# Performance work log

Measured on AMD Instinct MI355X. Metric: run time of the kernel, lower is better.

The kernel has to match this reference:

```python
import jax, jax.numpy as jnp
import numpy as np

N, NNODES, CIN, COUT = 64, 512, 32, 64


def setup_inputs() -> dict:
    key = jax.random.key(0)
    k1, k2, k3, k4, k5 = jax.random.split(key, 5)
    A = jax.random.normal(k1, (N, NNODES, NNODES), dtype=jnp.float32)
    X = jax.random.normal(k2, (N, NNODES, CIN), dtype=jnp.float32)
    A_coeffs = jax.random.normal(k3, (5 + 2 * CIN,), dtype=jnp.float32)
    x_num = 4 + 2 * CIN
    scale = np.sqrt(2.0) / (COUT + x_num)
    X_coeffs_1 = jax.random.normal(k4, (COUT, x_num), dtype=jnp.float32) * scale
    X_coeffs_2 = jax.random.normal(k5, (COUT, x_num), dtype=jnp.float32) * scale
    return {"A": A, "X": X, "A_coeffs": A_coeffs,
            "X_coeffs_1": X_coeffs_1, "X_coeffs_2": X_coeffs_2}


def _forward(A, X, A_coeffs, W1, W2):
    n = A.shape[-1]
    C = X.shape[-1]
    Xt = jnp.swapaxes(X, -1, -2)                      # N,C,n
    diag = jnp.diagonal(A, axis1=-2, axis2=-1)        # N,n
    mean_diag = diag.mean(-1)                         # N
    mean_cols = A.mean(-1)                            # N,n
    mean_all = mean_cols.mean(-1)                     # N
    mean_X = Xt.mean(-1)                              # N,C

    c = A_coeffs
    w6 = c[5:5 + C]                                   # coeffs for a6 (X_i + X_j)
    w7 = c[5 + C:5 + 2 * C]                           # coeffs for a7 (mean_X)
    # Fold the 'd,ndij->nij' contraction over the 7 basis tensors into
    # scalar/row/col broadcast terms (identical math, no N x (5+2C) x n x n tensor).
    s = jnp.einsum('c,nci->ni', w6, Xt)               # N,n
    const = c[1] * mean_all + c[2] * mean_diag + jnp.einsum('c,nc->n', w7, mean_X)
    vec = c[3] * mean_cols + c[4] * diag + s          # N,n
    A_t = c[0] * A + const[:, None, None] + vec[:, :, None] + vec[:, None, :]

    # X basis out_x: N x (4+2C) x n, order [x1, x2, x3, x4, x5, x6]
    ones_n = jnp.ones((1, 1, n), A.dtype)
    out_x = jnp.concatenate([
        Xt,                                           # x1: N,C,n
        mean_X[:, :, None] * ones_n,                  # x2: N,C,n
        mean_cols[:, None, :],                        # x3: N,1,n
        diag[:, None, :],                             # x4: N,1,n
        mean_diag[:, None, None] * ones_n,            # x5: N,1,n
        mean_all[:, None, None] * ones_n,             # x6: N,1,n
    ], axis=1)
    X1 = jnp.einsum('bd,ndi->nbi', W1, out_x)         # N,B,n
    X2 = jnp.einsum('bd,ndi->nbi', W2, out_x)         # N,B,n
    out = jnp.einsum('nij,nbj->nbi', A_t, X1) / n + X2  # N,B,n
    return jnp.swapaxes(out, -1, -2)                  # N,n,B


def reference(A, X, A_coeffs, X_coeffs_1, X_coeffs_2):
    return _forward(A, X, A_coeffs, X_coeffs_1, X_coeffs_2)
```

## Files before the change

kernel.cpp:

```cpp
#include <hip/hip_runtime.h>
#include <hip/hip_bf16.h>

#define NB 64
#define NN 512
#define CI 32
#define CO 64
#define XN 68

typedef __attribute__((ext_vector_type(8))) short bf16x8;
typedef __attribute__((ext_vector_type(4))) float f32x4;

__device__ inline short f2bf(float f) {
  union { __hip_bfloat16 h; unsigned short u; } cv;
  cv.h = __float2bfloat16(f);
  return (short)cv.u;
}

__device__ inline bf16x8 cvt8(float4 a, float4 b) {
  bf16x8 r;
  r[0] = f2bf(a.x); r[1] = f2bf(a.y); r[2] = f2bf(a.z); r[3] = f2bf(a.w);
  r[4] = f2bf(b.x); r[5] = f2bf(b.y); r[6] = f2bf(b.z); r[7] = f2bf(b.w);
  return r;
}

__device__ inline bf16x8 cvt8s(float4 a, float4 b, float s) {
  bf16x8 r;
  r[0] = f2bf(a.x * s); r[1] = f2bf(a.y * s); r[2] = f2bf(a.z * s); r[3] = f2bf(a.w * s);
  r[4] = f2bf(b.x * s); r[5] = f2bf(b.y * s); r[6] = f2bf(b.z * s); r[7] = f2bf(b.w * s);
  return r;
}

__global__ __launch_bounds__(256) void k1_rowstats(
    const float* __restrict__ A, float* __restrict__ mc, float* __restrict__ dg,
    float* __restrict__ pA, float* __restrict__ pD) {
  int b = blockIdx.x, ch = blockIdx.y;
  int t = threadIdx.x, w = t >> 6, lane = t & 63;
  int r0 = ch * 16;
  const float* Ab = A + (size_t)b * NN * NN;
  __shared__ float wsum[4];
  __shared__ float sD[16];
  float4 v0[4], v1[4];
#pragma unroll
  for (int m = 0; m < 4; ++m) {
    const float* rp = Ab + (size_t)(r0 + w * 4 + m) * NN;
    v0[m] = *(const float4*)(rp + lane * 4);
    v1[m] = *(const float4*)(rp + 256 + lane * 4);
  }
  float accR = 0.f;
#pragma unroll
  for (int m = 0; m < 4; ++m) {
    float s = (v0[m].x + v0[m].y) + (v0[m].z + v0[m].w) +
              (v1[m].x + v1[m].y) + (v1[m].z + v1[m].w);
#pragma unroll
    for (int off = 1; off < 64; off <<= 1) s += __shfl_xor(s, off, 64);
    if (lane == 0) mc[b * NN + r0 + w * 4 + m] = s * (1.0f / NN);
    accR += s;
  }
  if (lane == 0) wsum[w] = accR;
  if (t < 16) {
    float d = Ab[(size_t)(r0 + t) * NN + r0 + t];
    dg[b * NN + r0 + t] = d;
    sD[t] = d;
  }
  __syncthreads();
  if (t == 0) {
    pA[b * 32 + ch] = wsum[0] + wsum[1] + wsum[2] + wsum[3];
    float sd = 0.f;
#pragma unroll
    for (int k = 0; k < 16; ++k) sd += sD[k];
    pD[b * 32 + ch] = sd;
  }
}

__global__ __launch_bounds__(512) void k2_merged(
    const float* __restrict__ X, const float* __restrict__ cf,
    const float* __restrict__ W1, const float* __restrict__ W2,
    const float* __restrict__ mc, const float* __restrict__ dg,
    const float* __restrict__ pA, const float* __restrict__ pD,
    float* __restrict__ vplus, float* __restrict__ colv,
    unsigned short* __restrict__ X1) {
  int b = blockIdx.x, t = threadIdx.x;
  int w = t >> 6, lane = t & 63;
  __shared__ float sX[NN][36];
  __shared__ float sSv[NN];
  __shared__ float sMXp[16][32], sTCp[16][32];
  __shared__ float sWr[8][3];
  __shared__ float sc[69], mX[CI], tC[CI], sA1[CO];
  __shared__ float sS[6];

  if (t < 69) sc[t] = cf[t];
  const float* Xb = X + (size_t)b * NN * CI;
  float4 x4[8];
#pragma unroll
  for (int k = 0; k < 8; ++k) {
    x4[k] = *(const float4*)(Xb + (size_t)t * CI + k * 4);
    *(float4*)&sX[t][k * 4] = x4[k];
  }
  float mcj = mc[b * NN + t], dgj = dg[b * NN + t];
  __syncthreads();
  float sv = 0.f;
#pragma unroll
  for (int k = 0; k < 8; ++k) {
    sv += sc[5 + k * 4] * x4[k].x + sc[6 + k * 4] * x4[k].y +
          sc[7 + k * 4] * x4[k].z + sc[8 + k * 4] * x4[k].w;
  }
  float svec = fmaf(sc[3], mcj, fmaf(sc[4], dgj, sv));
  sSv[t] = svec;
  float p1 = svec, p2 = svec * mcj, p3 = svec * dgj;
#pragma unroll
  for (int off = 1; off < 64; off <<= 1) {
    p1 += __shfl_xor(p1, off, 64);
    p2 += __shfl_xor(p2, off, 64);
    p3 += __shfl_xor(p3, off, 64);
  }
  if (lane == 0) { sWr[w][0] = p1; sWr[w][1] = p2; sWr[w][2] = p3; }
  __syncthreads();
  {
    int c = lane & 31, rg = w * 2 + (lane >> 5);
    float s1 = 0.f, s2 = 0.f;
#pragma unroll
    for (int r = 0; r < 32; ++r) {
      int j = rg * 32 + r;
      float v = sX[j][c];
      s1 += v;
      s2 += sSv[j] * v;
    }
    sMXp[rg][c] = s1;
    sTCp[rg][c] = s2;
  }
  __syncthreads();
  if (t < 32) {
    float s1 = 0.f, s2 = 0.f;
#pragma unroll
    for (int g = 0; g < 16; ++g) { s1 += sMXp[g][t]; s2 += sTCp[g][t]; }
    mX[t] = s1 * (1.0f / NN);
    tC[t] = s2;
  } else if (t == 32) {
    float sA = 0.f, sD = 0.f;
#pragma unroll
    for (int k = 0; k < 32; ++k) { sA += pA[b * 32 + k]; sD += pD[b * 32 + k]; }
    sS[0] = sD * (1.0f / NN);
    sS[1] = sA * (1.0f / ((float)NN * (float)NN));
  } else if (t == 33) {
    float s1 = 0.f, s2 = 0.f, s3 = 0.f;
#pragma unroll
    for (int k = 0; k < 8; ++k) { s1 += sWr[k][0]; s2 += sWr[k][1]; s3 += sWr[k][2]; }
    sS[3] = s1; sS[4] = s2; sS[5] = s3;
  }
  __syncthreads();
  if (t == 0) {
    float s7 = 0.f;
#pragma unroll
    for (int c = 0; c < CI; ++c) s7 += sc[5 + CI + c] * mX[c];
    sS[2] = sc[1] * sS[1] + sc[2] * sS[0] + s7;
  }
  __syncthreads();
  vplus[b * NN + t] = sSv[t] + sS[2];
  if (t < CO) {
    int o = t;
    const float* w1 = W1 + o * XN;
    const float* w2 = W2 + o * XN;
    float w1mX = 0.f, a1 = 0.f, a2 = 0.f, wt = 0.f;
#pragma unroll
    for (int c = 0; c < CI; ++c) {
      w1mX += w1[c] * mX[c];
      a1 += w1[CI + c] * mX[c];
      a2 += w2[CI + c] * mX[c];
      wt += w1[c] * tC[c];
    }
    float smd = sS[0], sma = sS[1];
    a1 += w1[66] * smd + w1[67] * sma;
    a2 += w2[66] * smd + w2[67] * sma;
    float we0 = w1[64], we1 = w1[65];
    float S1n = w1mX + a1 + we0 * sma + we1 * smd;
    float SVn = (wt + a1 * sS[3] + we0 * sS[4] + we1 * sS[5]) * (1.0f / NN);
    sA1[o] = a1;
    float4 cvv = make_float4(S1n, a2 + SVn, w2[64], w2[65]);
    *(float4*)&colv[(b * CO + o) * 4] = cvv;
  }
  __syncthreads();
  {
    int ra = lane & 15, kg = lane >> 4, g = lane >> 4;
    bf16x8 wfrag[4];
    float ao[4], e0[4], e1[4];
#pragma unroll
    for (int to = 0; to < 4; ++to) {
      int o = to * 16 + ra;
      const float* wp = W1 + o * XN + kg * 8;
      wfrag[to] = cvt8(*(const float4*)wp, *(const float4*)(wp + 4));
      ao[to] = sA1[o];
      e0[to] = W1[o * XN + 64];
      e1[to] = W1[o * XN + 65];
    }
#pragma unroll
    for (int jj = 0; jj < 4; ++jj) {
      int j0 = w * 64 + jj * 16;
      const float* xp = &sX[j0 + ra][kg * 8];
      bf16x8 xf = cvt8(*(const float4*)xp, *(const float4*)(xp + 4));
      float4 mcv = *(const float4*)&mc[b * NN + j0 + g * 4];
      float4 dgv = *(const float4*)&dg[b * NN + j0 + g * 4];
      float mcr[4] = {mcv.x, mcv.y, mcv.z, mcv.w};
      float dgr[4] = {dgv.x, dgv.y, dgv.z, dgv.w};
#pragma unroll
      for (int to = 0; to < 4; ++to) {
        f32x4 zero = {0.f, 0.f, 0.f, 0.f};
        f32x4 d = __builtin_amdgcn_mfma_f32_16x16x32_bf16(xf, wfrag[to], zero, 0, 0, 0);
        union { unsigned short u[4]; uint2 v; } pk;
#pragma unroll
        for (int r = 0; r < 4; ++r) {
          float val = d[r] + ao[to] + e0[to] * mcr[r] + e1[to] * dgr[r];
          pk.u[r] = (unsigned short)f2bf(val);
        }
        *(uint2*)(X1 + ((size_t)b * CO + to * 16 + ra) * NN + j0 + g * 4) = pk.v;
      }
    }
  }
}

__global__ __launch_bounds__(512) void k5_mfma(
    const float* __restrict__ A, const unsigned short* __restrict__ X1,
    const float* __restrict__ X, const float* __restrict__ W2,
    const float* __restrict__ vplus, const float* __restrict__ mc,
    const float* __restrict__ dg, const float* __restrict__ colv,
    const float* __restrict__ cf, float* __restrict__ out) {
  int b = blockIdx.x, ic = blockIdx.y;
  int t = threadIdx.x, w = t >> 6, lane = t & 63;
  int ia = w & 1, q = w >> 1;
  int ra = lane & 15, kg = lane >> 4, g = lane >> 4;
  int i0 = ic * 32;
  __shared__ float sAcc[4 * 32 * 68];

  float c0n = cf[0] * (1.0f / NN);
  const float* Arow = A + ((size_t)(b * NN + i0 + ia * 16 + ra)) * NN;
  const unsigned short* X1b = X1 + (size_t)b * CO * NN;

  f32x4 acc[4] = {{0.f, 0.f, 0.f, 0.f}, {0.f, 0.f, 0.f, 0.f},
                  {0.f, 0.f, 0.f, 0.f}, {0.f, 0.f, 0.f, 0.f}};

#pragma unroll
  for (int jt = 0; jt < 4; ++jt) {
    int kb = q * 128 + jt * 32 + kg * 8;
    float4 a0 = *(const float4*)(Arow + kb);
    float4 a1 = *(const float4*)(Arow + kb + 4);
    bf16x8 af = cvt8s(a0, a1, c0n);
#pragma unroll
    for (int to = 0; to < 4; ++to) {
      bf16x8 bf = *(const bf16x8*)(X1b + (size_t)(to * 16 + ra) * NN + kb);
      acc[to] = __builtin_amdgcn_mfma_f32_16x16x32_bf16(af, bf, acc[to], 0, 0, 0);
    }
  }

  if (q == 0) {
    const float* xp = X + (size_t)(b * NN + i0 + ia * 16 + ra) * CI + kg * 8;
    bf16x8 xf = cvt8(*(const float4*)xp, *(const float4*)(xp + 4));
#pragma unroll
    for (int to = 0; to < 4; ++to) {
      const float* wp = W2 + (size_t)(to * 16 + ra) * XN + kg * 8;
      bf16x8 wf = cvt8(*(const float4*)wp, *(const float4*)(wp + 4));
      acc[to] = __builtin_amdgcn_mfma_f32_16x16x32_bf16(xf, wf, acc[to], 0, 0, 0);
    }
  }

  int ei = t >> 4, eo4 = (t & 15) * 4;
  float e_vp = vplus[b * NN + i0 + ei];
  float e_mc = mc[b * NN + i0 + ei];
  float e_dg = dg[b * NN + i0 + ei];
  float4 cv0 = *(const float4*)&colv[(b * CO + eo4 + 0) * 4];
  float4 cv1 = *(const float4*)&colv[(b * CO + eo4 + 1) * 4];
  float4 cv2 = *(const float4*)&colv[(b * CO + eo4 + 2) * 4];
  float4 cv3 = *(const float4*)&colv[(b * CO + eo4 + 3) * 4];

#pragma unroll
  for (int to = 0; to < 4; ++to)
#pragma unroll
    for (int r = 0; r < 4; ++r)
      sAcc[(q * 32 + ia * 16 + g * 4 + r) * 68 + to * 16 + ra] = acc[to][r];
  __syncthreads();

  {
    f32x4 s = {0.f, 0.f, 0.f, 0.f};
#pragma unroll
    for (int qq = 0; qq < 4; ++qq) s += *(const f32x4*)&sAcc[(qq * 32 + ei) * 68 + eo4];
    float4 res;
    res.x = s[0] + e_vp * cv0.x + cv0.y + e_mc * cv0.z + e_dg * cv0.w;
    res.y = s[1] + e_vp * cv1.x + cv1.y + e_mc * cv1.z + e_dg * cv1.w;
    res.z = s[2] + e_vp * cv2.x + cv2.y + e_mc * cv2.z + e_dg * cv2.w;
    res.w = s[3] + e_vp * cv3.x + cv3.y + e_mc * cv3.z + e_dg * cv3.w;
    *(float4*)&out[((size_t)(b * NN + i0 + ei)) * CO + eo4] = res;
  }
}

extern "C" void kernel_launch(void* const* d_in, const int* in_sizes, int n_in,
                              void* d_out, int out_size, void* d_ws, size_t ws_size,
                              hipStream_t stream) {
  const float* A = (const float*)d_in[0];
  const float* X = (const float*)d_in[1];
  const float* cf = (const float*)d_in[2];
  const float* W1 = (const float*)d_in[3];
  const float* W2 = (const float*)d_in[4];
  float* out = (float*)d_out;

  float* p = (float*)d_ws;
  float* mc = p;      p += NB * NN;
  float* dg = p;      p += NB * NN;
  float* vplus = p;   p += NB * NN;
  float* pA = p;      p += NB * 32;
  float* pD = p;      p += NB * 32;
  float* colv = p;    p += NB * CO * 4;
  unsigned short* X1 = (unsigned short*)p;

  k1_rowstats<<<dim3(NB, 32), 256, 0, stream>>>(A, mc, dg, pA, pD);
  k2_merged<<<NB, 512, 0, stream>>>(X, cf, W1, W2, mc, dg, pA, pD,
                                    vplus, colv, X1);
  k5_mfma<<<dim3(NB, 16), 512, 0, stream>>>(A, X1, X, W2, vplus, mc, dg,
                                            colv, cf, out);
}
```

Before: 55.71 us.

## Split X1 projection into separate kernel and fold mean/diag terms into extra MFMA rows

Moves the X·W1 MFMA projection out of the single-block-per-batch stats kernel into a new kernel with a 64x4 grid, so the projection no longer depends on the A row statistics. The mean_cols and diag contributions are no longer baked into X1. Instead they are stored as two extra bf16 rows of an extended Y buffer and contracted against A with one more MFMA per tile in the main kernel, then combined in the epilogue using per-output coefficients. The stats kernel now uses 1024 threads with shuffle reductions instead of LDS staging. This adds a fourth kernel launch and extra MFMA and global traffic for the padded rows.

New measurement: 68.89 us. 1.24x slower.

```diff
diff --git a/kernel.cpp b/kernel.cpp
--- a/kernel.cpp
+++ b/kernel.cpp
@@ -6,6 +6,7 @@
 #define CI 32
 #define CO 64
 #define XN 68
+#define YR 80
 
 typedef __attribute__((ext_vector_type(8))) short bf16x8;
 typedef __attribute__((ext_vector_type(4))) float f32x4;
@@ -72,61 +73,110 @@
   }
 }
 
-__global__ __launch_bounds__(512) void k2_merged(
+__global__ __launch_bounds__(256) void kY(
+    const float* __restrict__ X, const float* __restrict__ W1,
+    unsigned short* __restrict__ Yext) {
+  int b = blockIdx.x, yc = blockIdx.y;
+  int t = threadIdx.x, w = t >> 6, lane = t & 63;
+  int ra = lane & 15, kg = lane >> 4, g = lane >> 4;
+  const float* Xb = X + (size_t)b * NN * CI;
+
+  bf16x8 wfrag[4];
+#pragma unroll
+  for (int to = 0; to < 4; ++to) {
+    const float* wp = W1 + (to * 16 + ra) * XN + kg * 8;
+    wfrag[to] = cvt8(*(const float4*)wp, *(const float4*)(wp + 4));
+  }
+#pragma unroll
+  for (int jj = 0; jj < 2; ++jj) {
+    int j0 = yc * 128 + w * 32 + jj * 16;
+    const float* xp = Xb + (size_t)(j0 + ra) * CI + kg * 8;
+    bf16x8 xf = cvt8(*(const float4*)xp, *(const float4*)(xp + 4));
+#pragma unroll
+    for (int to = 0; to < 4; ++to) {
+      f32x4 zero = {0.f, 0.f, 0.f, 0.f};
+      f32x4 d = __builtin_amdgcn_mfma_f32_16x16x32_bf16(xf, wfrag[to], zero, 0, 0, 0);
+      union { unsigned short u[4]; uint2 v; } pk;
+#pragma unroll
+      for (int r = 0; r < 4; ++r) pk.u[r] = (unsigned short)f2bf(d[r]);
+      *(uint2*)(Yext + ((size_t)b * YR + to * 16 + ra) * NN + j0 + g * 4) = pk.v;
+    }
+  }
+  for (int idx = t; idx < 14 * 32; idx += 256) {
+    int row = 66 + (idx >> 5);
+    int c4 = (idx & 31) * 4;
+    *(uint2*)(Yext + ((size_t)b * YR + row) * NN + yc * 128 + c4) = make_uint2(0u, 0u);
+  }
+}
+
+__global__ __launch_bounds__(1024) void k2_stats(
     const float* __restrict__ X, const float* __restrict__ cf,
     const float* __restrict__ W1, const float* __restrict__ W2,
     const float* __restrict__ mc, const float* __restrict__ dg,
     const float* __restrict__ pA, const float* __restrict__ pD,
     float* __restrict__ vplus, float* __restrict__ colv,
-    unsigned short* __restrict__ X1) {
+    unsigned short* __restrict__ Yext) {
   int b = blockIdx.x, t = threadIdx.x;
   int w = t >> 6, lane = t & 63;
-  __shared__ float sX[NN][36];
-  __shared__ float sSv[NN];
-  __shared__ float sMXp[16][32], sTCp[16][32];
-  __shared__ float sWr[8][3];
-  __shared__ float sc[69], mX[CI], tC[CI], sA1[CO];
+  int h = t & 1, j = t >> 1;
+  __shared__ float sMXp[16][32], sTCp[16][32], sP[16][3];
+  __shared__ float sc[69], mX[CI], tC[CI];
   __shared__ float sS[6];
 
   if (t < 69) sc[t] = cf[t];
-  const float* Xb = X + (size_t)b * NN * CI;
-  float4 x4[8];
-#pragma unroll
-  for (int k = 0; k < 8; ++k) {
-    x4[k] = *(const float4*)(Xb + (size_t)t * CI + k * 4);
-    *(float4*)&sX[t][k * 4] = x4[k];
-  }
-  float mcj = mc[b * NN + t], dgj = dg[b * NN + t];
-  __syncthreads();
-  float sv = 0.f;
-#pragma unroll
-  for (int k = 0; k < 8; ++k) {
-    sv += sc[5 + k * 4] * x4[k].x + sc[6 + k * 4] * x4[k].y +
-          sc[7 + k * 4] * x4[k].z + sc[8 + k * 4] * x4[k].w;
-  }
-  float svec = fmaf(sc[3], mcj, fmaf(sc[4], dgj, sv));
-  sSv[t] = svec;
-  float p1 = svec, p2 = svec * mcj, p3 = svec * dgj;
+  const float* xp = X + ((size_t)b * NN + j) * CI + h * 16;
+  float4 x4[4];
+#pragma unroll
+  for (int k = 0; k < 4; ++k) x4[k] = *(const float4*)(xp + k * 4);
+  float mcj = mc[b * NN + j], dgj = dg[b * NN + j];
+  __syncthreads();
+
+  float up = 0.f;
+#pragma unroll
+  for (int k = 0; k < 4; ++k) {
+    int c0 = 5 + h * 16 + k * 4;
+    up += sc[c0] * x4[k].x + sc[c0 + 1] * x4[k].y +
+          sc[c0 + 2] * x4[k].z + sc[c0 + 3] * x4[k].w;
+  }
+  float u = up + __shfl_xor(up, 1, 64);
+  float vec = fmaf(sc[3], mcj, fmaf(sc[4], dgj, u));
+
+  float p1 = h ? 0.f : vec;
+  float p2 = h ? 0.f : vec * mcj;
+  float p3 = h ? 0.f : vec * dgj;
+  float4 t4[4];
+#pragma unroll
+  for (int k = 0; k < 4; ++k) {
+    t4[k].x = vec * x4[k].x; t4[k].y = vec * x4[k].y;
+    t4[k].z = vec * x4[k].z; t4[k].w = vec * x4[k].w;
+  }
 #pragma unroll
   for (int off = 1; off < 64; off <<= 1) {
     p1 += __shfl_xor(p1, off, 64);
     p2 += __shfl_xor(p2, off, 64);
     p3 += __shfl_xor(p3, off, 64);
   }
-  if (lane == 0) { sWr[w][0] = p1; sWr[w][1] = p2; sWr[w][2] = p3; }
-  __syncthreads();
-  {
-    int c = lane & 31, rg = w * 2 + (lane >> 5);
-    float s1 = 0.f, s2 = 0.f;
-#pragma unroll
-    for (int r = 0; r < 32; ++r) {
-      int j = rg * 32 + r;
-      float v = sX[j][c];
-      s1 += v;
-      s2 += sSv[j] * v;
-    }
-    sMXp[rg][c] = s1;
-    sTCp[rg][c] = s2;
+#pragma unroll
+  for (int off = 2; off < 64; off <<= 1) {
+#pragma unroll
+    for (int k = 0; k < 4; ++k) {
+      x4[k].x += __shfl_xor(x4[k].x, off, 64);
+      x4[k].y += __shfl_xor(x4[k].y, off, 64);
+      x4[k].z += __shfl_xor(x4[k].z, off, 64);
+      x4[k].w += __shfl_xor(x4[k].w, off, 64);
+      t4[k].x += __shfl_xor(t4[k].x, off, 64);
+      t4[k].y += __shfl_xor(t4[k].y, off, 64);
+      t4[k].z += __shfl_xor(t4[k].z, off, 64);
+      t4[k].w += __shfl_xor(t4[k].w, off, 64);
+    }
+  }
+  if (lane < 2) {
+#pragma unroll
+    for (int k = 0; k < 4; ++k) {
+      *(float4*)&sMXp[w][lane * 16 + k * 4] = x4[k];
+      *(float4*)&sTCp[w][lane * 16 + k * 4] = t4[k];
+    }
+    if (lane == 0) { sP[w][0] = p1; sP[w][1] = p2; sP[w][2] = p3; }
   }
   __syncthreads();
   if (t < 32) {
@@ -144,7 +194,7 @@
   } else if (t == 33) {
     float s1 = 0.f, s2 = 0.f, s3 = 0.f;
 #pragma unroll
-    for (int k = 0; k < 8; ++k) { s1 += sWr[k][0]; s2 += sWr[k][1]; s3 += sWr[k][2]; }
+    for (int k = 0; k < 16; ++k) { s1 += sP[k][0]; s2 += sP[k][1]; s3 += sP[k][2]; }
     sS[3] = s1; sS[4] = s2; sS[5] = s3;
   }
   __syncthreads();
@@ -155,7 +205,13 @@
     sS[2] = sc[1] * sS[1] + sc[2] * sS[0] + s7;
   }
   __syncthreads();
-  vplus[b * NN + t] = sSv[t] + sS[2];
+  if (h == 0) vplus[b * NN + j] = vec + sS[2];
+  if (t < NN) {
+    Yext[((size_t)b * YR + 64) * NN + t] = (unsigned short)f2bf(mc[b * NN + t]);
+  } else {
+    int t2 = t - NN;
+    Yext[((size_t)b * YR + 65) * NN + t2] = (unsigned short)f2bf(dg[b * NN + t2]);
+  }
   if (t < CO) {
     int o = t;
     const float* w1 = W1 + o * XN;
@@ -174,51 +230,15 @@
     float we0 = w1[64], we1 = w1[65];
     float S1n = w1mX + a1 + we0 * sma + we1 * smd;
     float SVn = (wt + a1 * sS[3] + we0 * sS[4] + we1 * sS[5]) * (1.0f / NN);
-    sA1[o] = a1;
-    float4 cvv = make_float4(S1n, a2 + SVn, w2[64], w2[65]);
-    *(float4*)&colv[(b * CO + o) * 4] = cvv;
-  }
-  __syncthreads();
-  {
-    int ra = lane & 15, kg = lane >> 4, g = lane >> 4;
-    bf16x8 wfrag[4];
-    float ao[4], e0[4], e1[4];
-#pragma unroll
-    for (int to = 0; to < 4; ++to) {
-      int o = to * 16 + ra;
-      const float* wp = W1 + o * XN + kg * 8;
-      wfrag[to] = cvt8(*(const float4*)wp, *(const float4*)(wp + 4));
-      ao[to] = sA1[o];
-      e0[to] = W1[o * XN + 64];
-      e1[to] = W1[o * XN + 65];
-    }
-#pragma unroll
-    for (int jj = 0; jj < 4; ++jj) {
-      int j0 = w * 64 + jj * 16;
-      const float* xp = &sX[j0 + ra][kg * 8];
-      bf16x8 xf = cvt8(*(const float4*)xp, *(const float4*)(xp + 4));
-      float4 mcv = *(const float4*)&mc[b * NN + j0 + g * 4];
-      float4 dgv = *(const float4*)&dg[b * NN + j0 + g * 4];
-      float mcr[4] = {mcv.x, mcv.y, mcv.z, mcv.w};
-      float dgr[4] = {dgv.x, dgv.y, dgv.z, dgv.w};
-#pragma unroll
-      for (int to = 0; to < 4; ++to) {
-        f32x4 zero = {0.f, 0.f, 0.f, 0.f};
-        f32x4 d = __builtin_amdgcn_mfma_f32_16x16x32_bf16(xf, wfrag[to], zero, 0, 0, 0);
-        union { unsigned short u[4]; uint2 v; } pk;
-#pragma unroll
-        for (int r = 0; r < 4; ++r) {
-          float val = d[r] + ao[to] + e0[to] * mcr[r] + e1[to] * dgr[r];
-          pk.u[r] = (unsigned short)f2bf(val);
-        }
-        *(uint2*)(X1 + ((size_t)b * CO + to * 16 + ra) * NN + j0 + g * 4) = pk.v;
-      }
-    }
+    float4 cva = make_float4(S1n, a2 + SVn, w2[64] + sc[0] * a1, w2[65]);
+    float4 cvb = make_float4(we0, we1, 0.f, 0.f);
+    *(float4*)&colv[(b * CO + o) * 8] = cva;
+    *(float4*)&colv[(b * CO + o) * 8 + 4] = cvb;
   }
 }
 
 __global__ __launch_bounds__(512) void k5_mfma(
-    const float* __restrict__ A, const unsigned short* __restrict__ X1,
+    const float* __restrict__ A, const unsigned short* __restrict__ Yext,
     const float* __restrict__ X, const float* __restrict__ W2,
     const float* __restrict__ vplus, const float* __restrict__ mc,
     const float* __restrict__ dg, const float* __restrict__ colv,
@@ -229,13 +249,15 @@
   int ra = lane & 15, kg = lane >> 4, g = lane >> 4;
   int i0 = ic * 32;
   __shared__ float sAcc[4 * 32 * 68];
+  __shared__ float sG[4 * 32 * 2];
 
   float c0n = cf[0] * (1.0f / NN);
   const float* Arow = A + ((size_t)(b * NN + i0 + ia * 16 + ra)) * NN;
-  const unsigned short* X1b = X1 + (size_t)b * CO * NN;
+  const unsigned short* Yb = Yext + (size_t)b * YR * NN;
 
   f32x4 acc[4] = {{0.f, 0.f, 0.f, 0.f}, {0.f, 0.f, 0.f, 0.f},
                   {0.f, 0.f, 0.f, 0.f}, {0.f, 0.f, 0.f, 0.f}};
+  f32x4 acc4 = {0.f, 0.f, 0.f, 0.f};
 
 #pragma unroll
   for (int jt = 0; jt < 4; ++jt) {
@@ -245,9 +267,11 @@
     bf16x8 af = cvt8s(a0, a1, c0n);
 #pragma unroll
     for (int to = 0; to < 4; ++to) {
-      bf16x8 bf = *(const bf16x8*)(X1b + (size_t)(to * 16 + ra) * NN + kb);
+      bf16x8 bf = *(const bf16x8*)(Yb + (size_t)(to * 16 + ra) * NN + kb);
       acc[to] = __builtin_amdgcn_mfma_f32_16x16x32_bf16(af, bf, acc[to], 0, 0, 0);
     }
+    bf16x8 bf4 = *(const bf16x8*)(Yb + (size_t)(64 + ra) * NN + kb);
+    acc4 = __builtin_amdgcn_mfma_f32_16x16x32_bf16(af, bf4, acc4, 0, 0, 0);
   }
 
   if (q == 0) {
@@ -265,27 +289,41 @@
   float e_vp = vplus[b * NN + i0 + ei];
   float e_mc = mc[b * NN + i0 + ei];
   float e_dg = dg[b * NN + i0 + ei];
-  float4 cv0 = *(const float4*)&colv[(b * CO + eo4 + 0) * 4];
-  float4 cv1 = *(const float4*)&colv[(b * CO + eo4 + 1) * 4];
-  float4 cv2 = *(const float4*)&colv[(b * CO + eo4 + 2) * 4];
-  float4 cv3 = *(const float4*)&colv[(b * CO + eo4 + 3) * 4];
+  float4 cva0 = *(const float4*)&colv[(b * CO + eo4 + 0) * 8];
+  float4 cvb0 = *(const float4*)&colv[(b * CO + eo4 + 0) * 8 + 4];
+  float4 cva1 = *(const float4*)&colv[(b * CO + eo4 + 1) * 8];
+  float4 cvb1 = *(const float4*)&colv[(b * CO + eo4 + 1) * 8 + 4];
+  float4 cva2 = *(const float4*)&colv[(b * CO + eo4 + 2) * 8];
+  float4 cvb2 = *(const float4*)&colv[(b * CO + eo4 + 2) * 8 + 4];
+  float4 cva3 = *(const float4*)&colv[(b * CO + eo4 + 3) * 8];
+  float4 cvb3 = *(const float4*)&colv[(b * CO + eo4 + 3) * 8 + 4];
 
 #pragma unroll
   for (int to = 0; to < 4; ++to)
 #pragma unroll
     for (int r = 0; r < 4; ++r)
       sAcc[(q * 32 + ia * 16 + g * 4 + r) * 68 + to * 16 + ra] = acc[to][r];
+  if (ra < 2) {
+#pragma unroll
+    for (int r = 0; r < 4; ++r)
+      sG[((q * 32 + ia * 16 + g * 4 + r) << 1) | ra] = acc4[r];
+  }
   __syncthreads();
 
   {
     f32x4 s = {0.f, 0.f, 0.f, 0.f};
-#pragma unroll
-    for (int qq = 0; qq < 4; ++qq) s += *(const f32x4*)&sAcc[(qq * 32 + ei) * 68 + eo4];
+    float Gm = 0.f, Gd = 0.f;
+#pragma unroll
+    for (int qq = 0; qq < 4; ++qq) {
+      s += *(const f32x4*)&sAcc[(qq * 32 + ei) * 68 + eo4];
+      Gm += sG[((qq * 32 + ei) << 1)];
+      Gd += sG[((qq * 32 + ei) << 1) | 1];
+    }
     float4 res;
-    res.x = s[0] + e_vp * cv0.x + cv0.y + e_mc * cv0.z + e_dg * cv0.w;
-    res.y = s[1] + e_vp * cv1.x + cv1.y + e_mc * cv1.z + e_dg * cv1.w;
-    res.z = s[2] + e_vp * cv2.x + cv2.y + e_mc * cv2.z + e_dg * cv2.w;
-    res.w = s[3] + e_vp * cv3.x + cv3.y + e_mc * cv3.z + e_dg * cv3.w;
+    res.x = s[0] + e_vp * cva0.x + cva0.y + e_mc * cva0.z + e_dg * cva0.w + Gm * cvb0.x + Gd * cvb0.y;
+    res.y = s[1] + e_vp * cva1.x + cva1.y + e_mc * cva1.z + e_dg * cva1.w + Gm * cvb1.x + Gd * cvb1.y;
+    res.z = s[2] + e_vp * cva2.x + cva2.y + e_mc * cva2.z + e_dg * cva2.w + Gm * cvb2.x + Gd * cvb2.y;
+    res.w = s[3] + e_vp * cva3.x + cva3.y + e_mc * cva3.z + e_dg * cva3.w + Gm * cvb3.x + Gd * cvb3.y;
     *(float4*)&out[((size_t)(b * NN + i0 + ei)) * CO + eo4] = res;
   }
 }
@@ -306,12 +344,13 @@
   float* vplus = p;   p += NB * NN;
   float* pA = p;      p += NB * 32;
   float* pD = p;      p += NB * 32;
-  float* colv = p;    p += NB * CO * 4;
-  unsigned short* X1 = (unsigned short*)p;
+  float* colv = p;    p += NB * CO * 8;
+  unsigned short* Yext = (unsigned short*)p;
 
   k1_rowstats<<<dim3(NB, 32), 256, 0, stream>>>(A, mc, dg, pA, pD);
-  k2_merged<<<NB, 512, 0, stream>>>(X, cf, W1, W2, mc, dg, pA, pD,
-                                    vplus, colv, X1);
-  k5_mfma<<<dim3(NB, 16), 512, 0, stream>>>(A, X1, X, W2, vplus, mc, dg,
+  kY<<<dim3(NB, 4), 256, 0, stream>>>(X, W1, Yext);
+  k2_stats<<<NB, 1024, 0, stream>>>(X, cf, W1, W2, mc, dg, pA, pD,
+                                    vplus, colv, Yext);
+  k5_mfma<<<dim3(NB, 16), 512, 0, stream>>>(A, Yext, X, W2, vplus, mc, dg,
                                             colv, cf, out);
 }
```
